# Kernel optimization log

Hardware: AMD Instinct MI355X
Metric: run time of the kernel (lower is better)

## Reference

```python
import jax, jax.numpy as jnp
import numpy as np

B, T, S, R, L = 16, 32, 512, 8, 256
H, E, V, NL = 512, 512, 50000, 3
OOV = 50


def setup_inputs() -> dict:
    key = jax.random.key(0)
    ks = jax.random.split(key, 40)
    p = lambda i, shape: jax.random.normal(ks[i], shape, dtype=jnp.float32) * 0.02
    d = {
        'tokens': jax.random.randint(ks[0], (B, T), 0, V),
        'src_oov': jax.random.randint(ks[1], (B, S), 0, V),
        'ref_oovs': jax.random.randint(ks[2], (B, R, L), 0, V),
        'src_mask': jnp.ones((B, S), bool),
        'ref_word_mask': jnp.ones((B, R, L), bool),
        'ref_doc_mask': jnp.ones((B, R), bool),
        'max_num_oov': OOV,
        'cur_word_rep': jax.random.normal(ks[3], (B, S, H), dtype=jnp.float32),
        'ref_word_reps': jax.random.normal(ks[4], (B, R, L, H), dtype=jnp.float32),
        'ref_doc_reps': jax.random.normal(ks[5], (B, R, H), dtype=jnp.float32),
        'hidden0': jax.random.normal(ks[6], (NL, B, H), dtype=jnp.float32),
        'embed_w': p(7, (V, E)),
        'gru_wih': p(8, (NL, 3 * H, H)),  # layer0 input dim E == H
        'gru_whh': p(9, (NL, 3 * H, H)),
        'gru_bih': p(10, (NL, 3 * H)),
        'gru_bhh': p(11, (NL, 3 * H)),
        'attn_Wd': p(12, (H, H)), 'attn_We': p(13, (H, H)), 'attn_v': p(14, (H,)),
        'hd_Wd': p(15, (H, H)), 'hd_We': p(16, (H, H)), 'hd_v': p(17, (H,)),
        'hw_Wd': p(18, (H, H)), 'hw_We': p(19, (H, H)), 'hw_v': p(20, (H,)),
        'gate_w': p(21, (2 * H, 1)), 'gate_b': p(22, (1,)),
        'fc_w': p(23, (2 * H, H)), 'fc_b': p(24, (H,)),
        'out_w': p(25, (H, V)), 'out_b': p(26, (V,)),
        'pgen_w': p(27, (E + 2 * H, 3)), 'pgen_b': p(28, (3,)),
    }
    return d


def _forward(embed_w, gru_wih, gru_whh, gru_bih, gru_bhh,
             attn_Wd, attn_We, attn_v, hd_Wd, hd_We, hd_v, hw_Wd, hw_We, hw_v,
             gate_w, gate_b, fc_w, fc_b, out_w, out_b, pgen_w, pgen_b,
             cur_word_rep, ref_word_reps, ref_doc_reps, hidden0,
             tokens, src_oov, ref_oovs, src_mask, ref_word_mask, ref_doc_mask,
             max_num_oov):
    b, t = tokens.shape
    x = embed_w[tokens]                               # [B,T,E]
    enc_proj = cur_word_rep @ attn_We                 # [B,S,H]
    doc_proj = ref_doc_reps @ hd_We                   # [B,R,H]
    word_proj = ref_word_reps @ hw_We                 # [B,R,L,H]
    NEG = jnp.float32(-1e9)

    def step(hidden, x_t):
        inp = x_t
        hs = []
        for l in range(hidden.shape[0]):
            gx = inp @ gru_wih[l].T + gru_bih[l]
            gh = hidden[l] @ gru_whh[l].T + gru_bhh[l]
            xr, xz, xn = jnp.split(gx, 3, -1)
            hr, hz, hn = jnp.split(gh, 3, -1)
            r = jax.nn.sigmoid(xr + hr)
            z = jax.nn.sigmoid(xz + hz)
            n = jnp.tanh(xn + r * hn)
            h = (1.0 - z) * n + z * hidden[l]
            hs.append(h)
            inp = h
        new_hidden = jnp.stack(hs)
        h_top = hs[-1]                                # [B,H]
        # additive attention over source words
        sc = jnp.tanh(enc_proj + (h_top @ attn_Wd)[:, None, :]) @ attn_v  # [B,S]
        aw = jax.nn.softmax(jnp.where(src_mask, sc, NEG), -1)
        ctx = jnp.einsum('bs,bsh->bh', aw, cur_word_rep)
        # hierarchical attention: doc level then word level
        scd = jnp.tanh(doc_proj + (h_top @ hd_Wd)[:, None, :]) @ hd_v     # [B,R]
        ad = jax.nn.softmax(jnp.where(ref_doc_mask, scd, NEG), -1)
        scw = jnp.tanh(word_proj + (h_top @ hw_Wd)[:, None, None, :]) @ hw_v  # [B,R,L]
        aww = jax.nn.softmax(jnp.where(ref_word_mask, scw, NEG), -1)
        ra = ad[:, :, None] * aww                     # [B,R,L]
        rctx = jnp.einsum('brl,brlh->bh', ra, ref_word_reps)
        # fusion gate
        g = jax.nn.sigmoid(jnp.concatenate([ctx, rctx], -1) @ gate_w + gate_b)  # [B,1]
        context = g * ctx + (1.0 - g) * rctx
        return new_hidden, (context, h_top, aw, ra)

    _, (contexts, hiddens, attn_dists, ref_attn_dists) = jax.lax.scan(
        step, hidden0, jnp.swapaxes(x, 0, 1))
    contexts = jnp.swapaxes(contexts, 0, 1)           # [B,T,H]
    hiddens = jnp.swapaxes(hiddens, 0, 1)             # [B,T,H]
    attn_dists = jnp.swapaxes(attn_dists, 0, 1)       # [B,T,S]
    ref_attn_dists = jnp.swapaxes(ref_attn_dists, 0, 1)  # [B,T,R,L]

    ch = jnp.concatenate([contexts, hiddens], -1)
    vocab_dist = jax.nn.softmax((ch @ fc_w + fc_b) @ out_w + out_b, -1)  # [B,T,V]
    pg = jax.nn.softmax(jnp.concatenate([contexts, hiddens, x], -1) @ pgen_w + pgen_b, -1)  # [B,T,3]
    vocab_dist_ = pg[..., 0:1] * vocab_dist
    attn_ = pg[..., 1:2] * attn_dists
    final = jnp.concatenate(
        [vocab_dist_, jnp.zeros((b, t, max_num_oov), vocab_dist_.dtype)], -1)
    bi = jnp.arange(b)[:, None, None]
    ti = jnp.arange(t)[None, :, None]
    idx = jnp.broadcast_to(src_oov[:, None, :], (b, t, src_oov.shape[-1]))
    final = final.at[bi, ti, idx].add(attn_)
    # multi-doc copy
    r, l = ref_oovs.shape[1], ref_oovs.shape[2]
    ref_attn_ = pg[..., 2][:, :, None, None] * ref_attn_dists
    ridx = jnp.broadcast_to(ref_oovs.reshape(b, 1, r * l), (b, t, r * l))
    final = final.at[bi, ti, ridx].add(ref_attn_.reshape(b, t, r * l))
    return final, attn_dists


def reference(tokens, src_oov, ref_oovs, src_mask, ref_word_mask, ref_doc_mask,
              max_num_oov, cur_word_rep, ref_word_reps, ref_doc_reps, hidden0,
              embed_w, gru_wih, gru_whh, gru_bih, gru_bhh,
              attn_Wd, attn_We, attn_v, hd_Wd, hd_We, hd_v, hw_Wd, hw_We, hw_v,
              gate_w, gate_b, fc_w, fc_b, out_w, out_b, pgen_w, pgen_b):
    return _forward(embed_w, gru_wih, gru_whh, gru_bih, gru_bhh,
                    attn_Wd, attn_We, attn_v, hd_Wd, hd_We, hd_v,
                    hw_Wd, hw_We, hw_v, gate_w, gate_b, fc_w, fc_b,
                    out_w, out_b, pgen_w, pgen_b,
                    cur_word_rep, ref_word_reps, ref_doc_reps, hidden0,
                    tokens, src_oov, ref_oovs, src_mask, ref_word_mask,
                    ref_doc_mask, max_num_oov)
```

## Files before the change

kernel.cpp:

```cpp
#include <hip/hip_runtime.h>
#include <hip/hip_bf16.h>


#define B_   16
#define T_   32
#define S_   512
#define R_   8
#define L_   256
#define RL_  2048
#define H_   512
#define V_   50000
#define NL_  3
#define OOV_ 50
#define M_   512
#define FINW 50050
#define S2C  2.8853900817779268f
#define GRUB 128
#define NCONV 128
#define HP16 520

typedef __attribute__((ext_vector_type(8))) short    short8;
typedef __attribute__((ext_vector_type(4))) float    f32x4;
typedef __attribute__((ext_vector_type(2))) _Float16 h2;
typedef __attribute__((ext_vector_type(8))) _Float16 h8;
// ... 265 lines not shown
  int cg = nb + cbase;
  long gbase = (long)(mb + rl) * FINW + cg;
  float mp = -1e30f;
  #pragma unroll 8
  for (int k = 0; k < 64; k += 2){
    float x0 = cbuf[rl][cbase + k], x1 = cbuf[rl][cbase + k + 1];
    float2 xy; xy.x = x0; xy.y = x1;
    *(float2*)(fin + gbase + k) = xy;
    if (cg + k < N)     mp = fmaxf(mp, x0);
    if (cg + k + 1 < N) mp = fmaxf(mp, x1);
  }
  float sp = 0.f;
  #pragma unroll 8
  for (int k = 0; k < 64; k++){
    if (cg + k < N) sp += __expf(cbuf[rl][cbase + k] - mp);
  }
  smx[rl][ch] = mp; ssx[rl][ch] = sp;
  __syncthreads();
  if (tid < 128){
    float ma = smx[tid][0], mb2 = smx[tid][1];
    float M = fmaxf(ma, mb2);
    float S = ssx[tid][0] * __expf(ma - M) + ssx[tid][1] * __expf(mb2 - M);
    long row = mb + tid;
    pm[row * 392 + blockIdx.y] = M;
    ps[row * 392 + blockIdx.y] = S;
  }
}


__global__ __launch_bounds__(512) void k_gru_mega(
    const float* __restrict__ gx0, const u16* __restrict__ wih_h,
    const u16* __restrict__ whh_h, const float* __restrict__ bih,
    const float* __restrict__ bhh, const float* __restrict__ hidden0,
    float* __restrict__ h_all, u16* __restrict__ ch_bf, unsigned int* cnt,
    const float* __restrict__ out_w, u16* __restrict__ outwT,
    const u16* __restrict__ cwr_bf, const u16* __restrict__ rwr_bf,
    const u16* __restrict__ rdr_bf, const u16* __restrict__ WT,
    u16* __restrict__ enc_bf, u16* __restrict__ wp_bf,
    float* __restrict__ doc_proj, int do_shadow){
  __shared__ u16 pH0[16][HP16], pH1[16][HP16], pX1[16][HP16], pH2[16][HP16], pX2[16][HP16];
  __shared__ float red0[8][3][4][16];
  __shared__ float red1[8][6][4][16];
  __shared__ float red2[8][6][4][16];
  __shared__ float tconv[2][32][33];
  int bid = blockIdx.x;
  int tid = threadIdx.x;

  if (bid >= GRUB){
    if (!do_shadow) return;
    int wid = bid - GRUB;
    int half = tid >> 8, t256 = tid & 255;
    int worker = wid * 2 + half;
    for (int tile = worker; tile < 1284; tile += 256){
      if (tile < 256)
        dev_gemm_tile(cwr_bf, H_, WT, H_, (const float*)0, (void*)enc_bf, H_,
                      H_, H_, 1, S2C, tile >> 2, tile & 3, t256);
      else if (tile < 1280){
        int t = tile - 256;
        dev_gemm_tile(rwr_bf, H_, WT + 2 * H_ * H_, H_, (const float*)0, (void*)wp_bf, H_,
                      H_, H_, 1, S2C, t >> 2, t & 3, t256);
      } else
        dev_gemm_tile(rdr_bf, H_, WT + H_ * H_, H_, (const float*)0, (void*)doc_proj, H_,
                      H_, H_, 0, S2C, 0, tile - 1280, t256);
    }
    __syncthreads();
    int sub = half, tx = t256 & 31, ty = t256 >> 5;
    const int NT = 1563 * 16;
    for (int base = wid * 2; base < NT; base += NCONV * 2){
      int tile = base + sub;
      bool act = tile < NT;
      int cx = act ? (tile % 1563) : 0;
      int ry = act ? (tile / 1563) : 0;
      int c0 = cx * 32, r0 = ry * 32;
      if (act){
        for (int i = ty; i < 32; i += 8){
          int c = c0 + tx;
          tconv[sub][i][tx] = (c < V_) ? out_w[(long)(r0 + i) * V_ + c] : 0.f;
        }
      }
      __syncthreads();
      if (act){
        for (int i = ty; i < 32; i += 8){
          int c = c0 + i;
          if (c < V_) outwT[(long)c * H_ + r0 + tx] = f2bf(tconv[sub][tx][i]);
        }
      }
      __syncthreads();
    }
    return;
  }

  int bx = bid;
  int b = tid & 15, jj = (tid >> 4) & 3, ks = tid >> 6;
  int j = bx * 4 + jj;
  int kbase = ks * 64;
  int srow = tid >> 5, sl32 = tid & 31;

  for (int s = 0; s < T_ + NL_ - 1; s++){
    int t0 = s, t1 = s - 1, t2v = s - 2;
    bool a0 = (t0 < T_);
    bool a1 = (t1 >= 0 && t1 < T_);
    bool a2 = (t2v >= 0 && t2v < T_);
    float hpj_r = 0.f, gx_r0 = 0.f, gx_r1 = 0.f, gx_r2 = 0.f;
    if (tid < 192){
      int lz = tid >> 6, b2 = tid & 15, jj2 = (tid >> 4) & 3;
      int j2 = bx * 4 + jj2;
      int tt = s - lz;
      if (tt >= 0 && tt < T_){
        hpj_r = (tt == 0) ? hidden0[(lz * B_ + b2) * H_ + j2]
                          : allcf(h_all + (long)((lz * T_ + tt - 1) * B_ + b2) * H_ + j2);
        if (lz == 0){
          const float* g = gx0 + (long)(b2 * T_ + tt) * 1536 + j2;
          gx_r0 = g[0]; gx_r1 = g[512]; gx_r2 = g[1024];
        }
      }
    }
    {
      u64 v;
      #define STAGE(PAN, ROWPTR, ATOMIC)                                         \
        {                                                                        \
          const u64* p = (const u64*)(ROWPTR);                                   \
          _Pragma("unroll")                                                      \
          for (int q = 0; q < 8; q++){                                           \
            v = (ATOMIC) ? allc(p + sl32 + 32 * q) : p[sl32 + 32 * q];           \
            union { u64 w; float f[2]; } uu; uu.w = v;                           \
            union { _Float16 h[2]; u32 u; } pk;                                  \
            pk.h[0] = (_Float16)uu.f[0]; pk.h[1] = (_Float16)uu.f[1];            \
            *(u32*)&PAN[srow][2 * (sl32 + 32 * q)] = pk.u;                       \
          }                                                                      \
        }
      if (a0){
        if (t0 == 0) STAGE(pH0, hidden0 + (long)(0 * B_ + srow) * H_, false)
        else         STAGE(pH0, h_all + (long)((0 * T_ + t0 - 1) * B_ + srow) * H_, true)
      }
      if (a1){
        if (t1 == 0) STAGE(pH1, hidden0 + (long)(1 * B_ + srow) * H_, false)
        else         STAGE(pH1, h_all + (long)((1 * T_ + t1 - 1) * B_ + srow) * H_, true)
        STAGE(pX1, h_all + (long)((0 * T_ + t1) * B_ + srow) * H_, true)
      }
      if (a2){
        if (t2v == 0) STAGE(pH2, hidden0 + (long)(2 * B_ + srow) * H_, false)
        else          STAGE(pH2, h_all + (long)((2 * T_ + t2v - 1) * B_ + srow) * H_, true)
        STAGE(pX2, h_all + (long)((1 * T_ + t2v) * B_ + srow) * H_, true)
      }
      #undef STAGE
    }
    __syncthreads();

    if (a0){
      const u16* wl = whh_h;
      const h8* w0 = (const h8*)(wl + ((long)(0 * H_ + j)) * H_ + kbase);
      const h8* w1 = (const h8*)(wl + ((long)(1 * H_ + j)) * H_ + kbase);
      const h8* w2 = (const h8*)(wl + ((long)(2 * H_ + j)) * H_ + kbase);
      float s0 = 0.f, s1 = 0.f, s2 = 0.f;
      #pragma unroll 2
      for (int k8 = 0; k8 < 8; k8++){
        h8 hv = *(const h8*)&pH0[b][kbase + 8 * k8];
        s0 = dot8h(w0[k8], hv, s0);
        s1 = dot8h(w1[k8], hv, s1);
        s2 = dot8h(w2[k8], hv, s2);
      }
      red0[ks][0][jj][b] = s0; red0[ks][1][jj][b] = s1; red0[ks][2][jj][b] = s2;
    }
    if (a1){
      const u16* wl = whh_h + (long)1 * 1536 * H_;
      const u16* ul = wih_h + (long)1 * 1536 * H_;
      const h8* w0 = (const h8*)(wl + ((long)(0 * H_ + j)) * H_ + kbase);
      const h8* w1 = (const h8*)(wl + ((long)(1 * H_ + j)) * H_ + kbase);
      const h8* w2 = (const h8*)(wl + ((long)(2 * H_ + j)) * H_ + kbase);
      const h8* u0 = (const h8*)(ul + ((long)(0 * H_ + j)) * H_ + kbase);
      const h8* u1 = (const h8*)(ul + ((long)(1 * H_ + j)) * H_ + kbase);
      const h8* u2 = (const h8*)(ul + ((long)(2 * H_ + j)) * H_ + kbase);
      float s0 = 0.f, s1 = 0.f, s2 = 0.f, x0 = 0.f, x1 = 0.f, x2 = 0.f;
      #pragma unroll 2
      for (int k8 = 0; k8 < 8; k8++){
        h8 hv = *(const h8*)&pH1[b][kbase + 8 * k8];
        h8 xv = *(const h8*)&pX1[b][kbase + 8 * k8];
        s0 = dot8h(w0[k8], hv, s0);
        s1 = dot8h(w1[k8], hv, s1);
        s2 = dot8h(w2[k8], hv, s2);
        x0 = dot8h(u0[k8], xv, x0);
        x1 = dot8h(u1[k8], xv, x1);
        x2 = dot8h(u2[k8], xv, x2);
      }
      red1[ks][0][jj][b] = s0; red1[ks][1][jj][b] = s1; red1[ks][2][jj][b] = s2;
      red1[ks][3][jj][b] = x0; red1[ks][4][jj][b] = x1; red1[ks][5][jj][b] = x2;
    }
    if (a2){
      const u16* wl = whh_h + (long)2 * 1536 * H_;
      const u16* ul = wih_h + (long)2 * 1536 * H_;
      const h8* w0 = (const h8*)(wl + ((long)(0 * H_ + j)) * H_ + kbase);
      const h8* w1 = (const h8*)(wl + ((long)(1 * H_ + j)) * H_ + kbase);
      const h8* w2 = (const h8*)(wl + ((long)(2 * H_ + j)) * H_ + kbase);
      const h8* u0 = (const h8*)(ul + ((long)(0 * H_ + j)) * H_ + kbase);
      const h8* u1 = (const h8*)(ul + ((long)(1 * H_ + j)) * H_ + kbase);
      const h8* u2 = (const h8*)(ul + ((long)(2 * H_ + j)) * H_ + kbase);
      float s0 = 0.f, s1 = 0.f, s2 = 0.f, x0 = 0.f, x1 = 0.f, x2 = 0.f;
      #pragma unroll 2
      for (int k8 = 0; k8 < 8; k8++){
        h8 hv = *(const h8*)&pH2[b][kbase + 8 * k8];
        h8 xv = *(const h8*)&pX2[b][kbase + 8 * k8];
        s0 = dot8h(w0[k8], hv, s0);
        s1 = dot8h(w1[k8], hv, s1);
        s2 = dot8h(w2[k8], hv, s2);
        x0 = dot8h(u0[k8], xv, x0);
        x1 = dot8h(u1[k8], xv, x1);
        x2 = dot8h(u2[k8], xv, x2);
      }
      red2[ks][0][jj][b] = s0; red2[ks][1][jj][b] = s1; red2[ks][2][jj][b] = s2;
      red2[ks][3][jj][b] = x0; red2[ks][4][jj][b] = x1; red2[ks][5][jj][b] = x2;
    }
    __syncthreads();

    if (tid < 192){
      int lz = tid >> 6, b2 = tid & 15, jj2 = (tid >> 4) & 3;
      int j2 = bx * 4 + jj2;
      int tt = s - lz;
      if (tt >= 0 && tt < T_){
        float gh[3], gxv[3];
        #pragma unroll
        for (int g = 0; g < 3; g++){
          float a = 0.f, c = 0.f;
          if (lz == 0){
            #pragma unroll
            for (int q = 0; q < 8; q++) a += red0[q][g][jj2][b2];
          } else if (lz == 1){
            #pragma unroll
            for (int q = 0; q < 8; q++){ a += red1[q][g][jj2][b2]; c += red1[q][3 + g][jj2][b2]; }
          } else {
            #pragma unroll
            for (int q = 0; q < 8; q++){ a += red2[q][g][jj2][b2]; c += red2[q][3 + g][jj2][b2]; }
          }
          gh[g] = a + bhh[lz * 1536 + g * H_ + j2];
          if (lz == 0) gxv[g] = (g == 0) ? gx_r0 : (g == 1) ? gx_r1 : gx_r2;
          else         gxv[g] = c + bih[lz * 1536 + g * H_ + j2];
        }
        float r = sigmoid_(gxv[0] + gh[0]);
        float z = sigmoid_(gxv[1] + gh[1]);
        float n = tanh_(gxv[2] + r * gh[2]);
        float h = (1.f - z) * n + z * hpj_r;
        union { float f; u32 u; } cv; cv.f = h;
        __hip_atomic_store((u32*)(h_all + (long)((lz * T_ + tt) * B_ + b2) * H_ + j2),
                           cv.u, __ATOMIC_RELAXED, __HIP_MEMORY_SCOPE_AGENT);
        if (lz == 2) ch_bf[(long)(b2 * T_ + tt) * 1024 + 512 + j2] = f2bf(h);
      }
    }
    if (s == T_ + NL_ - 2) break;

    __syncthreads();
    if (tid == 0)
      __hip_atomic_store(cnt + bx * 16, (u32)(s + 1),
                         __ATOMIC_RELAXED, __HIP_MEMORY_SCOPE_AGENT);
    if (tid < GRUB){
      long guard = 0;
      while (__hip_atomic_load(cnt + tid * 16, __ATOMIC_RELAXED, __HIP_MEMORY_SCOPE_AGENT)
               < (u32)(s + 1) && guard < (1L << 23)){
        __builtin_amdgcn_s_sleep(1);
        guard++;
      }
    }
    __syncthreads();
  }
}


__global__ __launch_bounds__(256) void k_scores2(const u16* __restrict__ enc,
    const u16* __restrict__ wp, const float* __restrict__ dec_all,
    const float* __restrict__ av, const float* __restrict__ wv,
    float* __restrict__ aw, float* __restrict__ ra){
  int b = blockIdx.x, y = blockIdx.y, tz = blockIdx.z;
  const u16* ebf; int erpb, doff, et, ldo; const float* vv; float* out;
  if (y < 8){ ebf = enc; erpb = S_;  doff = 0;    vv = av; out = aw; ldo = S_;  et = y; }
  else      { ebf = wp;  erpb = RL_; doff = 1024; vv = wv; out = ra; ldo = RL_; et = y - 8; }
  int tid = threadIdx.x;
  __shared__ float dsh[8][512];
  __shared__ float vsh[512];
  __shared__ float redsv[4];
  for (int i = tid; i < 8 * 128; i += 256){
    int tl = i >> 7, c = (i & 127) << 2;
    *(f32x4*)&dsh[tl][c] =
      *(const f32x4*)(dec_all + ((long)(b * T_) + tz * 8 + tl) * 1536 + doff + c);
  }
  for (int i = tid; i < 128; i += 256)
    *(f32x4*)&vsh[i << 2] = *(const f32x4*)(vv + (i << 2));
  __syncthreads();
  float pvv = vsh[tid] + vsh[tid + 256];
  for (int o = 32; o > 0; o >>= 1) pvv += __shfl_xor(pvv, o);
  if ((tid & 63) == 0) redsv[tid >> 6] = pvv;
  __syncthreads();
// ... 71 lines not shown
    if (tid == 0){
      float m = -1e30f;
      for (int q = 0; q < 8; q++) m = fmaxf(m, red8[q][0]);
      float e[8], sum = 0.f;
      for (int q = 0; q < 8; q++){ e[q] = __expf(red8[q][0] - m); sum += e[q]; }
      float inv = 1.f / sum;
      for (int q = 0; q < 8; q++) ad[rid * R_ + q] = e[q] * inv;
    }
  }
}

__global__ __launch_bounds__(256) void k_aww_ra(float* __restrict__ raBuf,
                                                const float* __restrict__ ad){
  int rid = blockIdx.x, r = blockIdx.y, tid = threadIdx.x;
  float* row = raBuf + (long)rid * RL_ + r * L_;
  float x = row[tid];
  float m = x;
  for (int o = 32; o > 0; o >>= 1) m = fmaxf(m, __shfl_xor(m, o));
  __shared__ float red[4];
  if ((tid & 63) == 0) red[tid >> 6] = m;
  __syncthreads();
  m = fmaxf(fmaxf(red[0], red[1]), fmaxf(red[2], red[3]));
  float e = __expf(x - m);
  float s = e;
  for (int o = 32; o > 0; o >>= 1) s += __shfl_xor(s, o);
  __syncthreads();
  if ((tid & 63) == 0) red[tid >> 6] = s;
  __syncthreads();
  s = red[0] + red[1] + red[2] + red[3];
  row[tid] = (e / s) * ad[rid * R_ + r];
}


__global__ __launch_bounds__(256) void k_awgemm(const float* __restrict__ wts, int KS, int CH,
    const u16* __restrict__ Wbuf, float* __restrict__ pdst){
  int b = blockIdx.x, ht = blockIdx.y, kc = blockIdx.z;
  int tid = threadIdx.x;
  int hl = tid & 63, tq = tid >> 6;
  int h = ht * 256 + hl * 4;
  int base = kc * CH;
  float a[8][4];
  #pragma unroll
  for (int tt = 0; tt < 8; tt++)
    #pragma unroll
    for (int q = 0; q < 4; q++) a[tt][q] = 0.f;
  const float* wrow = wts + ((long)(b * T_) + tq * 8) * KS + base;
  for (int sl = 0; sl < CH; sl++){
    const u16* wp = Wbuf + ((long)b * KS + base + sl) * H_ + h;
    u32 p0 = *(const u32*)(wp);
    u32 p1 = *(const u32*)(wp + 2);
    float v0 = bf2f((u16)(p0 & 0xffff)), v1 = bf2f((u16)(p0 >> 16));
    float v2 = bf2f((u16)(p1 & 0xffff)), v3 = bf2f((u16)(p1 >> 16));
    #pragma unroll
    for (int tt = 0; tt < 8; tt++){
      float w = wrow[(long)tt * KS + sl];
      a[tt][0] += w * v0; a[tt][1] += w * v1;
      a[tt][2] += w * v2; a[tt][3] += w * v3;
    }
  }
  #pragma unroll
  for (int tt = 0; tt < 8; tt++){
    long o = (long)kc * (2 * M_ * H_) + ((long)(b * T_ + tq * 8 + tt)) * H_ + h;
    *(f32x4*)(pdst + o) = (f32x4){a[tt][0], a[tt][1], a[tt][2], a[tt][3]};
  }
}

__global__ __launch_bounds__(256) void k_red8(const float* __restrict__ pbuf,
                                              float* __restrict__ outp){
  long n = 2L * M_ * H_;
// ... 28 lines not shown
    contexts[(long)rid * H_ + h] = v;
    ch_bf[(long)rid * 1024 + h] = f2bf(v);
  }
  float p0 = 0.f, p1 = 0.f, p2 = 0.f;
  for (int k = tid; k < 1536; k += 256){
    float v;
    if (k < 512)       v = g * c[k] + (1.f - g) * rc[k];
    else if (k < 1024) v = h_all[((2 * T_ + t) * B_ + b) * H_ + (k - 512)];
    else               v = bf2f(x_bf[(long)rid * H_ + (k - 1024)]);
    p0 += v * pgen_w[k * 3 + 0];
    p1 += v * pgen_w[k * 3 + 1];
    p2 += v * pgen_w[k * 3 + 2];
  }
  for (int o = 32; o > 0; o >>= 1){
    p0 += __shfl_xor(p0, o); p1 += __shfl_xor(p1, o); p2 += __shfl_xor(p2, o);
  }
  __shared__ float r0[4], r1[4], r2[4];
  if ((tid & 63) == 0){ r0[tid >> 6] = p0; r1[tid >> 6] = p1; r2[tid >> 6] = p2; }
  __syncthreads();
  if (tid == 0){
    p0 = r0[0]+r0[1]+r0[2]+r0[3] + pgen_b[0];
    p1 = r1[0]+r1[1]+r1[2]+r1[3] + pgen_b[1];
    p2 = r2[0]+r2[1]+r2[2]+r2[3] + pgen_b[2];
    float m = fmaxf(p0, fmaxf(p1, p2));
    float e0 = __expf(p0 - m), e1 = __expf(p1 - m), e2 = __expf(p2 - m);
    float inv = 1.f / (e0 + e1 + e2);
    pg[rid * 3 + 0] = e0 * inv;
    pg[rid * 3 + 1] = e1 * inv;
    pg[rid * 3 + 2] = e2 * inv;
  }
}


__global__ __launch_bounds__(256) void k_vred391(const float* __restrict__ pm,
    const float* __restrict__ ps, float* __restrict__ vmax, float* __restrict__ vsum){
  int rid = blockIdx.x, tid = threadIdx.x;
  const float* mrow = pm + (long)rid * 392;
  const float* srow = ps + (long)rid * 392;
  float m = -1e30f, s = 0.f;
  for (int q = tid; q < 391; q += 256){
    float m2 = mrow[q], s2 = srow[q];
    float M = fmaxf(m, m2);
    s = s * __expf(m - M) + s2 * __expf(m2 - M);
    m = M;
  }
  for (int o = 32; o > 0; o >>= 1){
    float m2 = __shfl_xor(m, o), s2 = __shfl_xor(s, o);
    float M = fmaxf(m, m2);
    s = s * __expf(m - M) + s2 * __expf(m2 - M);
    m = M;
  }
  __shared__ float rm[4], rs[4];
  if ((tid & 63) == 0){ rm[tid >> 6] = m; rs[tid >> 6] = s; }
  __syncthreads();
  if (tid == 0){
    float Mx = rm[0], Sx = rs[0];
    for (int q = 1; q < 4; q++){
      float M2 = fmaxf(Mx, rm[q]);
      Sx = Sx * __expf(Mx - M2) + rs[q] * __expf(rm[q] - M2);
      Mx = M2;
    }
    vmax[rid] = Mx; vsum[rid] = Sx;
  }
}

__global__ __launch_bounds__(256) void k_final_vocab(float* __restrict__ fin,
    const float* __restrict__ vmax, const float* __restrict__ vsum,
    const float* __restrict__ pg){
  int rid = blockIdx.y;
  int v = (blockIdx.x * 256 + threadIdx.x) * 2;
  if (v >= FINW) return;
  long base = (long)rid * FINW;
  float scale = pg[rid * 3 + 0] / vsum[rid];
  float mx = vmax[rid];
  if (v + 1 < V_){
    float2* p = (float2*)(fin + base + v);
    float2 x = *p;
    x.x = __expf(x.x - mx) * scale;
    x.y = __expf(x.y - mx) * scale;
    *p = x;
  } else {
    for (int q = 0; q < 2 && v + q < FINW; q++){
      float x = fin[base + v + q];
      fin[base + v + q] = (v + q < V_) ? __expf(x - mx) * scale : 0.f;
    }
  }
}

__global__ __launch_bounds__(256) void k_scatter_src(float* __restrict__ fin,
    const float* __restrict__ aw, const float* __restrict__ pg,
    const int* __restrict__ src_oov){
  int rid = blockIdx.x, tid = threadIdx.x;
  int b = rid / T_;
  float p1 = pg[rid * 3 + 1];
  for (int s = tid; s < S_; s += 256){
    float val = p1 * aw[(long)rid * S_ + s];
    int idx = src_oov[b * S_ + s];
    atomicAdd(fin + (long)rid * FINW + idx, val);
  }
}

__global__ __launch_bounds__(256) void k_scatter_ref(float* __restrict__ fin,
    const float* __restrict__ raBuf, const float* __restrict__ pg,
    const int* __restrict__ ref_oovs){
  int rid = blockIdx.x, tid = threadIdx.x;
  int b = rid / T_;
  float p2 = pg[rid * 3 + 2];
  for (int i = tid; i < RL_; i += 256){
    float val = p2 * raBuf[(long)rid * RL_ + i];
    int idx = ref_oovs[b * RL_ + i];
    atomicAdd(fin + (long)rid * FINW + idx, val);
  }
}


extern "C" void kernel_launch(void* const* d_in, const int* in_sizes, int n_in,
                              void* d_out, int out_size, void* d_ws, size_t ws_size,
                              hipStream_t stream)
{
  (void)in_sizes; (void)n_in; (void)out_size;
  const int*   tokens   = (const int*)  d_in[0];
  const int*   src_oov  = (const int*)  d_in[1];
  const int*   ref_oovs = (const int*)  d_in[2];
  const float* cwr      = (const float*)d_in[7];
  const float* rwr      = (const float*)d_in[8];
  const float* rdr      = (const float*)d_in[9];
  const float* hidden0  = (const float*)d_in[10];
  const float* embed_w  = (const float*)d_in[11];
  const float* gru_wih  = (const float*)d_in[12];
  const float* gru_whh  = (const float*)d_in[13];
  const float* gru_bih  = (const float*)d_in[14];
  const float* gru_bhh  = (const float*)d_in[15];
  const float* attn_Wd  = (const float*)d_in[16];
  const float* attn_We  = (const float*)d_in[17];
  const float* attn_v   = (const float*)d_in[18];
  const float* hd_Wd    = (const float*)d_in[19];
  const float* hd_We    = (const float*)d_in[20];
  const float* hd_v     = (const float*)d_in[21];
  const float* hw_Wd    = (const float*)d_in[22];
  const float* hw_We    = (const float*)d_in[23];
  const float* hw_v     = (const float*)d_in[24];
  const float* gate_w   = (const float*)d_in[25];
  const float* gate_b   = (const float*)d_in[26];
  const float* fc_w     = (const float*)d_in[27];
  const float* fc_b     = (const float*)d_in[28];
  const float* out_w    = (const float*)d_in[29];
  const float* out_b    = (const float*)d_in[30];
  const float* pgen_w   = (const float*)d_in[31];
  const float* pgen_b   = (const float*)d_in[32];

  float* fin = (float*)d_out;
  float* aw  = fin + (long)M_ * FINW;

  char* wptr = (char*)d_ws;
  auto alloc = [&](size_t nbytes) -> void* {
    void* p = (void*)wptr;
    wptr += (nbytes + 255) & ~(size_t)255;
    return p;
  };
  float* gx0      = (float*)alloc((size_t)M_ * 1536 * 4);
  float* h_all    = (float*)alloc((size_t)NL_ * T_ * B_ * H_ * 4);
  float* dec_all  = (float*)alloc((size_t)M_ * 1536 * 4);
  float* raBuf    = (float*)alloc((size_t)M_ * RL_ * 4);
  float* ad       = (float*)alloc((size_t)M_ * R_ * 4);
  float* ctx      = (float*)alloc((size_t)M_ * H_ * 4);
  float* rctx     = (float*)alloc((size_t)M_ * H_ * 4);
  float* contexts = (float*)alloc((size_t)M_ * H_ * 4);
  float* pg       = (float*)alloc((size_t)M_ * 3 * 4);
  float* vmax     = (float*)alloc((size_t)M_ * 4);
  float* vsum     = (float*)alloc((size_t)M_ * 4);
  float* pm       = (float*)alloc((size_t)M_ * 392 * 4);
  float* ps       = (float*)alloc((size_t)M_ * 392 * 4);
  float* doc_proj = (float*)alloc((size_t)B_ * R_ * H_ * 4);
  float* pbuf     = (float*)alloc((size_t)8 * 2 * M_ * H_ * 4);
  unsigned int* gru_cnt = (unsigned int*)alloc(GRUB * 16 * 4);
  u16* x_bf       = (u16*)alloc((size_t)M_ * H_ * 2);
  u16* ch_bf      = (u16*)alloc((size_t)M_ * 1024 * 2);
  u16* whh_h16    = (u16*)alloc((size_t)NL_ * 1536 * H_ * 2);
  u16* wih_h16    = (u16*)alloc((size_t)NL_ * 1536 * H_ * 2);
  u16* wih0_bf    = (u16*)alloc((size_t)1536 * H_ * 2);
  u16* WT         = (u16*)alloc((size_t)6 * H_ * H_ * 2);
  u16* fcwT       = (u16*)alloc((size_t)H_ * 1024 * 2);
  u16* fcout_bf   = (u16*)alloc((size_t)M_ * H_ * 2);
  u16* cwr_bf     = (u16*)alloc((size_t)B_ * S_ * H_ * 2);
  u16* enc_bf     = (u16*)alloc((size_t)B_ * S_ * H_ * 2);
  u16* rwr_bf     = (u16*)alloc((size_t)B_ * RL_ * H_ * 2);
  u16* wp_bf      = (u16*)alloc((size_t)B_ * RL_ * H_ * 2);
  u16* rdr_bf     = (u16*)alloc((size_t)B_ * R_ * H_ * 2);
  u16* outwT_ded  = (u16*)alloc((size_t)V_ * H_ * 2);
  bool big = ((char*)outwT_ded + (size_t)V_ * H_ * 2) <= ((char*)d_ws + ws_size);
  u16* outwT = big ? outwT_ded : rwr_bf;
  int nshadow = big ? NCONV : 0;

  hipMemsetAsync(gru_cnt, 0, GRUB * 16 * 4, stream);

  k_embed<<<M_, 256, 0, stream>>>(tokens, embed_w, x_bf);
  {
    CJ j0{cwr, cwr_bf, (long)B_ * S_ * H_, 0};
    CJ j1{rwr, rwr_bf, (long)B_ * RL_ * H_, 0};
    CJ j2{gru_whh, whh_h16, (long)NL_ * 1536 * H_, 1};
    CJ j3{gru_wih, wih_h16, (long)NL_ * 1536 * H_, 1};
    CJ j4{rdr, rdr_bf, (long)B_ * R_ * H_, 0};
    CJ j5{gru_wih, wih0_bf, (long)1536 * H_, 0};
    k_conv6<<<dim3(512, 6), 256, 0, stream>>>(j0, j1, j2, j3, j4, j5);
  }
  k_convT6<<<dim3(16, 16, 6), 256, 0, stream>>>(attn_We, hd_We, hw_We,
                                                attn_Wd, hd_Wd, hw_Wd, WT);
  k_convT<<<dim3(16, 32), 256, 0, stream>>>(fc_w, 1024, H_, fcwT);

  k_gemm_nt<<<dim3(4, 12), 256, 0, stream>>>(x_bf, H_, wih0_bf, H_, gru_bih,
                                             (void*)gx0, 1536, 1536, H_, 0, 1.f);
  if (!big){
    k_gemm_nt<<<dim3(64, 4), 256, 0, stream>>>(cwr_bf, H_, WT, H_, (const float*)0,
                                               (void*)enc_bf, H_, H_, H_, 1, S2C);
    k_gemm_nt<<<dim3(256, 4), 256, 0, stream>>>(rwr_bf, H_, WT + 2 * H_ * H_, H_, (const float*)0,
                                                (void*)wp_bf, H_, H_, H_, 1, S2C);
    k_gemm_nt<<<dim3(1, 4), 256, 0, stream>>>(rdr_bf, H_, WT + H_ * H_, H_, (const float*)0,
                                              (void*)doc_proj, H_, H_, H_, 0, S2C);
  }

  k_gru_mega<<<GRUB + nshadow, 512, 0, stream>>>(gx0, wih_h16, whh_h16, gru_bih, gru_bhh,
                                                 hidden0, h_all, ch_bf, gru_cnt,
                                                 out_w, outwT, cwr_bf, rwr_bf, rdr_bf,
                                                 WT, enc_bf, wp_bf, doc_proj, big ? 1 : 0);

  k_gemm_nt<<<dim3(4, 12), 256, 0, stream>>>(ch_bf + 512, 1024, WT + 3 * H_ * H_, H_,
                                             (const float*)0, (void*)dec_all, 1536, 1536, H_, 0, S2C);

  k_scores2<<<dim3(16, 40, 4), 256, 0, stream>>>(enc_bf, wp_bf, dec_all, attn_v, hw_v, aw, raBuf);
  k_smax_scd<<<dim3(M_, 2), 256, 0, stream>>>(aw, doc_proj, dec_all, hd_v, ad);
  k_aww_ra<<<dim3(M_, R_), 256, 0, stream>>>(raBuf, ad);

  k_awgemm<<<dim3(B_, 2, 8), 256, 0, stream>>>(aw, S_, 64, cwr_bf, pbuf);
  k_awgemm<<<dim3(B_, 2, 8), 256, 0, stream>>>(raBuf, RL_, 256, rwr_bf, pbuf + (long)M_ * H_);
  if (!big)
    k_convT<<<dim3(1563, 16), 256, 0, stream>>>(out_w, H_, V_, outwT);
  k_red8<<<(2 * M_ * H_ + 255) / 256, 256, 0, stream>>>(pbuf, ctx);

  k_gatepgen<<<M_, 256, 0, stream>>>(ctx, rctx, gate_w, gate_b, contexts, ch_bf,
                                     h_all, x_bf, pgen_w, pgen_b, pg);

  k_gemm_nt<<<dim3(4, 4), 256, 0, stream>>>(ch_bf, 1024, fcwT, 1024, fc_b,
                                            (void*)fcout_bf, H_, H_, 1024, 1, 1.f);
  k_gemm_out<<<dim3(4, 391), 256, 0, stream>>>(fcout_bf, outwT, out_b, fin, pm, ps);
  k_vred391<<<M_, 256, 0, stream>>>(pm, ps, vmax, vsum);
  k_final_vocab<<<dim3(98, M_), 256, 0, stream>>>(fin, vmax, vsum, pg);
  k_scatter_src<<<M_, 256, 0, stream>>>(fin, aw, pg, src_oov);
  k_scatter_ref<<<M_, 256, 0, stream>>>(fin, raBuf, pg, ref_oovs);
}
```

Before: 1.148 ms.

## Restructure GRU megakernel reduction, stage fp16 hidden states, and fuse tail kernels

The GRU persistent kernel now stores an fp16 copy of each hidden state so the next step can stage it into LDS without converting, and it reuses the layer-below panel as the input operand. The split-K reduction moves from a shared-memory reduce plus a second barrier to warp shuffles, and the biases are hoisted into registers. Each polling thread now checks two counters instead of one. Separately, the two awgemm launches are merged into one, vocab max/sum reduction is folded into k_final_vocab (each of its 98 blocks per row recomputes the reduction), and the two scatter kernels are merged. These changes cut per-step barrier and conversion latency on the recurrent critical path and reduce launch count, at the cost of redundant reductions and extra fp16 stores.

```diff
diff --git a/kernel.cpp b/kernel.cpp
--- a/kernel.cpp
+++ b/kernel.cpp
@@ -321,16 +321,14 @@
     const float* __restrict__ gx0, const u16* __restrict__ wih_h,
     const u16* __restrict__ whh_h, const float* __restrict__ bih,
     const float* __restrict__ bhh, const float* __restrict__ hidden0,
-    float* __restrict__ h_all, u16* __restrict__ ch_bf, unsigned int* cnt,
+    float* __restrict__ h_all, u16* __restrict__ h16,
+    u16* __restrict__ ch_bf, unsigned int* cnt,
     const float* __restrict__ out_w, u16* __restrict__ outwT,
     const u16* __restrict__ cwr_bf, const u16* __restrict__ rwr_bf,
     const u16* __restrict__ rdr_bf, const u16* __restrict__ WT,
     u16* __restrict__ enc_bf, u16* __restrict__ wp_bf,
     float* __restrict__ doc_proj, int do_shadow){
-  __shared__ u16 pH0[16][HP16], pH1[16][HP16], pX1[16][HP16], pH2[16][HP16], pX2[16][HP16];
-  __shared__ float red0[8][3][4][16];
-  __shared__ float red1[8][6][4][16];
-  __shared__ float red2[8][6][4][16];
+  __shared__ u16 P0[16][HP16], P1[16][HP16], P2[16][HP16];
   __shared__ float tconv[2][32][33];
   int bid = blockIdx.x;
   int tid = threadIdx.x;
@@ -380,76 +378,109 @@
   }
 
   int bx = bid;
-  int b = tid & 15, jj = (tid >> 4) & 3, ks = tid >> 6;
+  int jj = tid >> 7, b = (tid >> 3) & 15, ks = tid & 7;
   int j = bx * 4 + jj;
   int kbase = ks * 64;
   int srow = tid >> 5, sl32 = tid & 31;
+
+  float bh00 = 0, bh01 = 0, bh02 = 0, bh10 = 0, bh11 = 0, bh12 = 0,
+        bh20 = 0, bh21 = 0, bh22 = 0, bi10 = 0, bi11 = 0, bi12 = 0,
+        bi20 = 0, bi21 = 0, bi22 = 0;
+  if (ks == 0){
+    bh00 = bhh[0 * 1536 + 0 * H_ + j]; bh01 = bhh[0 * 1536 + 1 * H_ + j];
+    bh02 = bhh[0 * 1536 + 2 * H_ + j];
+    bh10 = bhh[1 * 1536 + 0 * H_ + j]; bh11 = bhh[1 * 1536 + 1 * H_ + j];
+    bh12 = bhh[1 * 1536 + 2 * H_ + j];
+    bh20 = bhh[2 * 1536 + 0 * H_ + j]; bh21 = bhh[2 * 1536 + 1 * H_ + j];
+    bh22 = bhh[2 * 1536 + 2 * H_ + j];
+    bi10 = bih[1 * 1536 + 0 * H_ + j]; bi11 = bih[1 * 1536 + 1 * H_ + j];
+    bi12 = bih[1 * 1536 + 2 * H_ + j];
+    bi20 = bih[2 * 1536 + 0 * H_ + j]; bi21 = bih[2 * 1536 + 1 * H_ + j];
+    bi22 = bih[2 * 1536 + 2 * H_ + j];
+  }
 
   for (int s = 0; s < T_ + NL_ - 1; s++){
     int t0 = s, t1 = s - 1, t2v = s - 2;
     bool a0 = (t0 < T_);
     bool a1 = (t1 >= 0 && t1 < T_);
     bool a2 = (t2v >= 0 && t2v < T_);
-    float hpj_r = 0.f, gx_r0 = 0.f, gx_r1 = 0.f, gx_r2 = 0.f;
-    if (tid < 192){
-      int lz = tid >> 6, b2 = tid & 15, jj2 = (tid >> 4) & 3;
-      int j2 = bx * 4 + jj2;
-      int tt = s - lz;
-      if (tt >= 0 && tt < T_){
-        hpj_r = (tt == 0) ? hidden0[(lz * B_ + b2) * H_ + j2]
-                          : allcf(h_all + (long)((lz * T_ + tt - 1) * B_ + b2) * H_ + j2);
-        if (lz == 0){
-          const float* g = gx0 + (long)(b2 * T_ + tt) * 1536 + j2;
-          gx_r0 = g[0]; gx_r1 = g[512]; gx_r2 = g[1024];
+    float hp0 = 0.f, hp1 = 0.f, hp2 = 0.f, g0r = 0.f, g1r = 0.f, g2r = 0.f;
+    if (ks == 0){
+      if (a0){
+        hp0 = (t0 == 0) ? hidden0[(0 * B_ + b) * H_ + j]
+                        : allcf(h_all + (long)((0 * T_ + t0 - 1) * B_ + b) * H_ + j);
+        const float* g = gx0 + (long)(b * T_ + t0) * 1536 + j;
+        g0r = g[0]; g1r = g[512]; g2r = g[1024];
+      }
+      if (a1) hp1 = (t1 == 0) ? hidden0[(1 * B_ + b) * H_ + j]
+                              : allcf(h_all + (long)((1 * T_ + t1 - 1) * B_ + b) * H_ + j);
+      if (a2) hp2 = (t2v == 0) ? hidden0[(2 * B_ + b) * H_ + j]
+                               : allcf(h_all + (long)((2 * T_ + t2v - 1) * B_ + b) * H_ + j);
+    }
+    if (a0 && t0 == 0){
+      const f32x4* p = (const f32x4*)(hidden0 + (long)(0 * B_ + srow) * H_);
+      #pragma unroll
+      for (int q = 0; q < 4; q++){
+        f32x4 v = p[sl32 + 32 * q];
+        u64 pk = (u64)f2h(v[0]) | ((u64)f2h(v[1]) << 16)
+               | ((u64)f2h(v[2]) << 32) | ((u64)f2h(v[3]) << 48);
+        *(u64*)&P0[srow][4 * (sl32 + 32 * q)] = pk;
+      }
+    } else if (a0 || a1){
+      const u64* p = (const u64*)(h16 + ((long)(0 * T_ + s - 1) * B_ + srow) * H_);
+      #pragma unroll
+      for (int q = 0; q < 4; q++)
+        *(u64*)&P0[srow][4 * (sl32 + 32 * q)] = allc(p + sl32 + 32 * q);
+    }
+    if (a1 && t1 == 0){
+      const f32x4* p = (const f32x4*)(hidden0 + (long)(1 * B_ + srow) * H_);
+      #pragma unroll
+      for (int q = 0; q < 4; q++){
+        f32x4 v = p[sl32 + 32 * q];
+        u64 pk = (u64)f2h(v[0]) | ((u64)f2h(v[1]) << 16)
+               | ((u64)f2h(v[2]) << 32) | ((u64)f2h(v[3]) << 48);
+        *(u64*)&P1[srow][4 * (sl32 + 32 * q)] = pk;
+      }
+    } else if (a1 || a2){
+      const u64* p = (const u64*)(h16 + ((long)(1 * T_ + s - 2) * B_ + srow) * H_);
+      #pragma unroll
+      for (int q = 0; q < 4; q++)
+        *(u64*)&P1[srow][4 * (sl32 + 32 * q)] = allc(p + sl32 + 32 * q);
+    }
+    if (a2){
+      if (t2v == 0){
+        const f32x4* p = (const f32x4*)(hidden0 + (long)(2 * B_ + srow) * H_);
+        #pragma unroll
+        for (int q = 0; q < 4; q++){
+          f32x4 v = p[sl32 + 32 * q];
+          u64 pk = (u64)f2h(v[0]) | ((u64)f2h(v[1]) << 16)
+                 | ((u64)f2h(v[2]) << 32) | ((u64)f2h(v[3]) << 48);
+          *(u64*)&P2[srow][4 * (sl32 + 32 * q)] = pk;
         }
-      }
-    }
-    {
-      u64 v;
-      #define STAGE(PAN, ROWPTR, ATOMIC)                                         \
-        {                                                                        \
-          const u64* p = (const u64*)(ROWPTR);                                   \
-          _Pragma("unroll")                                                      \
-          for (int q = 0; q < 8; q++){                                           \
-            v = (ATOMIC) ? allc(p + sl32 + 32 * q) : p[sl32 + 32 * q];           \
-            union { u64 w; float f[2]; } uu; uu.w = v;                           \
-            union { _Float16 h[2]; u32 u; } pk;                                  \
-            pk.h[0] = (_Float16)uu.f[0]; pk.h[1] = (_Float16)uu.f[1];            \
-            *(u32*)&PAN[srow][2 * (sl32 + 32 * q)] = pk.u;                       \
-          }                                                                      \
-        }
-      if (a0){
-        if (t0 == 0) STAGE(pH0, hidden0 + (long)(0 * B_ + srow) * H_, false)
-        else         STAGE(pH0, h_all + (long)((0 * T_ + t0 - 1) * B_ + srow) * H_, true)
-      }
-      if (a1){
-        if (t1 == 0) STAGE(pH1, hidden0 + (long)(1 * B_ + srow) * H_, false)
-        else         STAGE(pH1, h_all + (long)((1 * T_ + t1 - 1) * B_ + srow) * H_, true)
-        STAGE(pX1, h_all + (long)((0 * T_ + t1) * B_ + srow) * H_, true)
-      }
-      if (a2){
-        if (t2v == 0) STAGE(pH2, hidden0 + (long)(2 * B_ + srow) * H_, false)
-        else          STAGE(pH2, h_all + (long)((2 * T_ + t2v - 1) * B_ + srow) * H_, true)
-        STAGE(pX2, h_all + (long)((1 * T_ + t2v) * B_ + srow) * H_, true)
-      }
-      #undef STAGE
+      } else {
+        const u64* p = (const u64*)(h16 + ((long)(2 * T_ + s - 3) * B_ + srow) * H_);
+        #pragma unroll
+        for (int q = 0; q < 4; q++)
+          *(u64*)&P2[srow][4 * (sl32 + 32 * q)] = allc(p + sl32 + 32 * q);
+      }
     }
     __syncthreads();
 
+    float A0 = 0, A1 = 0, A2 = 0;
+    float Bh0 = 0, Bh1 = 0, Bh2 = 0, Bx0 = 0, Bx1 = 0, Bx2 = 0;
+    float Ch0 = 0, Ch1 = 0, Ch2 = 0, Cx0 = 0, Cx1 = 0, Cx2 = 0;
     if (a0){
       const u16* wl = whh_h;
       const h8* w0 = (const h8*)(wl + ((long)(0 * H_ + j)) * H_ + kbase);
       const h8* w1 = (const h8*)(wl + ((long)(1 * H_ + j)) * H_ + kbase);
       const h8* w2 = (const h8*)(wl + ((long)(2 * H_ + j)) * H_ + kbase);
-      float s0 = 0.f, s1 = 0.f, s2 = 0.f;
       #pragma unroll 2
       for (int k8 = 0; k8 < 8; k8++){
-        h8 hv = *(const h8*)&pH0[b][kbase + 8 * k8];
-        s0 = dot8h(w0[k8], hv, s0);
-        s1 = dot8h(w1[k8], hv, s1);
-        s2 = dot8h(w2[k8], hv, s2);
-      }
-      red0[ks][0][jj][b] = s0; red0[ks][1][jj][b] = s1; red0[ks][2][jj][b] = s2;
+        h8 hv = *(const h8*)&P0[b][kbase + 8 * k8];
+        A0 = dot8h(w0[k8], hv, A0);
+        A1 = dot8h(w1[k8], hv, A1);
+        A2 = dot8h(w2[k8], hv, A2);
+      }
     }
     if (a1){
       const u16* wl = whh_h + (long)1 * 1536 * H_;
@@ -460,20 +491,17 @@
       const h8* u0 = (const h8*)(ul + ((long)(0 * H_ + j)) * H_ + kbase);
       const h8* u1 = (const h8*)(ul + ((long)(1 * H_ + j)) * H_ + kbase);
       const h8* u2 = (const h8*)(ul + ((long)(2 * H_ + j)) * H_ + kbase);
-      float s0 = 0.f, s1 = 0.f, s2 = 0.f, x0 = 0.f, x1 = 0.f, x2 = 0.f;
       #pragma unroll 2
       for (int k8 = 0; k8 < 8; k8++){
-        h8 hv = *(const h8*)&pH1[b][kbase + 8 * k8];
-        h8 xv = *(const h8*)&pX1[b][kbase + 8 * k8];
-        s0 = dot8h(w0[k8], hv, s0);
-        s1 = dot8h(w1[k8], hv, s1);
-        s2 = dot8h(w2[k8], hv, s2);
-        x0 = dot8h(u0[k8], xv, x0);
-        x1 = dot8h(u1[k8], xv, x1);
-        x2 = dot8h(u2[k8], xv, x2);
-      }
-      red1[ks][0][jj][b] = s0; red1[ks][1][jj][b] = s1; red1[ks][2][jj][b] = s2;
-      red1[ks][3][jj][b] = x0; red1[ks][4][jj][b] = x1; red1[ks][5][jj][b] = x2;
+        h8 hv = *(const h8*)&P1[b][kbase + 8 * k8];
+        h8 xv = *(const h8*)&P0[b][kbase + 8 * k8];
+        Bh0 = dot8h(w0[k8], hv, Bh0);
+        Bh1 = dot8h(w1[k8], hv, Bh1);
+        Bh2 = dot8h(w2[k8], hv, Bh2);
+        Bx0 = dot8h(u0[k8], xv, Bx0);
+        Bx1 = dot8h(u1[k8], xv, Bx1);
+        Bx2 = dot8h(u2[k8], xv, Bx2);
+      }
     }
     if (a2){
       const u16* wl = whh_h + (long)2 * 1536 * H_;
@@ -484,54 +512,58 @@
       const h8* u0 = (const h8*)(ul + ((long)(0 * H_ + j)) * H_ + kbase);
       const h8* u1 = (const h8*)(ul + ((long)(1 * H_ + j)) * H_ + kbase);
       const h8* u2 = (const h8*)(ul + ((long)(2 * H_ + j)) * H_ + kbase);
-      float s0 = 0.f, s1 = 0.f, s2 = 0.f, x0 = 0.f, x1 = 0.f, x2 = 0.f;
       #pragma unroll 2
       for (int k8 = 0; k8 < 8; k8++){
-        h8 hv = *(const h8*)&pH2[b][kbase + 8 * k8];
-        h8 xv = *(const h8*)&pX2[b][kbase + 8 * k8];
-        s0 = dot8h(w0[k8], hv, s0);
-        s1 = dot8h(w1[k8], hv, s1);
-        s2 = dot8h(w2[k8], hv, s2);
-        x0 = dot8h(u0[k8], xv, x0);
-        x1 = dot8h(u1[k8], xv, x1);
-        x2 = dot8h(u2[k8], xv, x2);
-      }
-      red2[ks][0][jj][b] = s0; red2[ks][1][jj][b] = s1; red2[ks][2][jj][b] = s2;
-      red2[ks][3][jj][b] = x0; red2[ks][4][jj][b] = x1; red2[ks][5][jj][b] = x2;
-    }
-    __syncthreads();
-
-    if (tid < 192){
-      int lz = tid >> 6, b2 = tid & 15, jj2 = (tid >> 4) & 3;
-      int j2 = bx * 4 + jj2;
-      int tt = s - lz;
-      if (tt >= 0 && tt < T_){
-        float gh[3], gxv[3];
-        #pragma unroll
-        for (int g = 0; g < 3; g++){
-          float a = 0.f, c = 0.f;
-          if (lz == 0){
-            #pragma unroll
-            for (int q = 0; q < 8; q++) a += red0[q][g][jj2][b2];
-          } else if (lz == 1){
-            #pragma unroll
-            for (int q = 0; q < 8; q++){ a += red1[q][g][jj2][b2]; c += red1[q][3 + g][jj2][b2]; }
-          } else {
-            #pragma unroll
-            for (int q = 0; q < 8; q++){ a += red2[q][g][jj2][b2]; c += red2[q][3 + g][jj2][b2]; }
-          }
-          gh[g] = a + bhh[lz * 1536 + g * H_ + j2];
-          if (lz == 0) gxv[g] = (g == 0) ? gx_r0 : (g == 1) ? gx_r1 : gx_r2;
-          else         gxv[g] = c + bih[lz * 1536 + g * H_ + j2];
-        }
-        float r = sigmoid_(gxv[0] + gh[0]);
-        float z = sigmoid_(gxv[1] + gh[1]);
-        float n = tanh_(gxv[2] + r * gh[2]);
-        float h = (1.f - z) * n + z * hpj_r;
+        h8 hv = *(const h8*)&P2[b][kbase + 8 * k8];
+        h8 xv = *(const h8*)&P1[b][kbase + 8 * k8];
+        Ch0 = dot8h(w0[k8], hv, Ch0);
+        Ch1 = dot8h(w1[k8], hv, Ch1);
+        Ch2 = dot8h(w2[k8], hv, Ch2);
+        Cx0 = dot8h(u0[k8], xv, Cx0);
+        Cx1 = dot8h(u1[k8], xv, Cx1);
+        Cx2 = dot8h(u2[k8], xv, Cx2);
+      }
+    }
+    #define RED3(v) { v += __shfl_xor(v, 1); v += __shfl_xor(v, 2); v += __shfl_xor(v, 4); }
+    if (a0){ RED3(A0) RED3(A1) RED3(A2) }
+    if (a1){ RED3(Bh0) RED3(Bh1) RED3(Bh2) RED3(Bx0) RED3(Bx1) RED3(Bx2) }
+    if (a2){ RED3(Ch0) RED3(Ch1) RED3(Ch2) RED3(Cx0) RED3(Cx1) RED3(Cx2) }
+    #undef RED3
+
+    if (ks == 0){
+      if (a0){
+        float r = sigmoid_(g0r + A0 + bh00);
+        float z = sigmoid_(g1r + A1 + bh01);
+        float n = tanh_(g2r + r * (A2 + bh02));
+        float h = (1.f - z) * n + z * hp0;
         union { float f; u32 u; } cv; cv.f = h;
-        __hip_atomic_store((u32*)(h_all + (long)((lz * T_ + tt) * B_ + b2) * H_ + j2),
+        __hip_atomic_store((u32*)(h_all + (long)((0 * T_ + t0) * B_ + b) * H_ + j),
                            cv.u, __ATOMIC_RELAXED, __HIP_MEMORY_SCOPE_AGENT);
-        if (lz == 2) ch_bf[(long)(b2 * T_ + tt) * 1024 + 512 + j2] = f2bf(h);
+        __hip_atomic_store(h16 + ((long)(0 * T_ + t0) * B_ + b) * H_ + j,
+                           f2h(h), __ATOMIC_RELAXED, __HIP_MEMORY_SCOPE_AGENT);
+      }
+      if (a1){
+        float r = sigmoid_(Bx0 + bi10 + Bh0 + bh10);
+        float z = sigmoid_(Bx1 + bi11 + Bh1 + bh11);
+        float n = tanh_(Bx2 + bi12 + r * (Bh2 + bh12));
+        float h = (1.f - z) * n + z * hp1;
+        union { float f; u32 u; } cv; cv.f = h;
+        __hip_atomic_store((u32*)(h_all + (long)((1 * T_ + t1) * B_ + b) * H_ + j),
+                           cv.u, __ATOMIC_RELAXED, __HIP_MEMORY_SCOPE_AGENT);
+        __hip_atomic_store(h16 + ((long)(1 * T_ + t1) * B_ + b) * H_ + j,
+                           f2h(h), __ATOMIC_RELAXED, __HIP_MEMORY_SCOPE_AGENT);
+      }
+      if (a2){
+        float r = sigmoid_(Cx0 + bi20 + Ch0 + bh20);
+        float z = sigmoid_(Cx1 + bi21 + Ch1 + bh21);
+        float n = tanh_(Cx2 + bi22 + r * (Ch2 + bh22));
+        float h = (1.f - z) * n + z * hp2;
+        union { float f; u32 u; } cv; cv.f = h;
+        __hip_atomic_store((u32*)(h_all + (long)((2 * T_ + t2v) * B_ + b) * H_ + j),
+                           cv.u, __ATOMIC_RELAXED, __HIP_MEMORY_SCOPE_AGENT);
+        __hip_atomic_store(h16 + ((long)(2 * T_ + t2v) * B_ + b) * H_ + j,
+                           f2h(h), __ATOMIC_RELAXED, __HIP_MEMORY_SCOPE_AGENT);
+        ch_bf[(long)(b * T_ + t2v) * 1024 + 512 + j] = f2bf(h);
       }
     }
     if (s == T_ + NL_ - 2) break;
@@ -540,10 +572,12 @@
     if (tid == 0)
       __hip_atomic_store(cnt + bx * 16, (u32)(s + 1),
                          __ATOMIC_RELAXED, __HIP_MEMORY_SCOPE_AGENT);
-    if (tid < GRUB){
+    if (tid < 64){
       long guard = 0;
-      while (__hip_atomic_load(cnt + tid * 16, __ATOMIC_RELAXED, __HIP_MEMORY_SCOPE_AGENT)
-               < (u32)(s + 1) && guard < (1L << 23)){
+      while ((__hip_atomic_load(cnt + tid * 16, __ATOMIC_RELAXED, __HIP_MEMORY_SCOPE_AGENT)
+                < (u32)(s + 1) ||
+              __hip_atomic_load(cnt + (tid + 64) * 16, __ATOMIC_RELAXED, __HIP_MEMORY_SCOPE_AGENT)
+                < (u32)(s + 1)) && guard < (1L << 23)){
         __builtin_amdgcn_s_sleep(1);
         guard++;
       }
@@ -681,9 +715,13 @@
 }
 
 
-__global__ __launch_bounds__(256) void k_awgemm(const float* __restrict__ wts, int KS, int CH,
-    const u16* __restrict__ Wbuf, float* __restrict__ pdst){
-  int b = blockIdx.x, ht = blockIdx.y, kc = blockIdx.z;
+__global__ __launch_bounds__(256) void k_awgemm2(const float* __restrict__ aw,
+    const float* __restrict__ raBuf, const u16* __restrict__ cwr_bf,
+    const u16* __restrict__ rwr_bf, float* __restrict__ pbuf){
+  int b = blockIdx.x, ht = blockIdx.y, z = blockIdx.z;
+  const float* wts; const u16* Wbuf; float* pdst; int KS, CH, kc;
+  if (z < 8){ wts = aw;    Wbuf = cwr_bf; pdst = pbuf;                 KS = S_;  CH = 64;  kc = z; }
+  else      { wts = raBuf; Wbuf = rwr_bf; pdst = pbuf + (long)M_ * H_; KS = RL_; CH = 256; kc = z - 8; }
   int tid = threadIdx.x;
   int hl = tid & 63, tq = tid >> 6;
   int h = ht * 256 + hl * 4;
@@ -778,9 +816,10 @@
 }
 
 
-__global__ __launch_bounds__(256) void k_vred391(const float* __restrict__ pm,
-    const float* __restrict__ ps, float* __restrict__ vmax, float* __restrict__ vsum){
-  int rid = blockIdx.x, tid = threadIdx.x;
+__global__ __launch_bounds__(256) void k_final_vocab(float* __restrict__ fin,
+    const float* __restrict__ pm, const float* __restrict__ ps,
+    const float* __restrict__ pg){
+  int rid = blockIdx.y, tid = threadIdx.x;
   const float* mrow = pm + (long)rid * 392;
   const float* srow = ps + (long)rid * 392;
   float m = -1e30f, s = 0.f;
@@ -796,7 +835,7 @@
     s = s * __expf(m - M) + s2 * __expf(m2 - M);
     m = M;
   }
-  __shared__ float rm[4], rs[4];
+  __shared__ float rm[4], rs[4], fm, fs;
   if ((tid & 63) == 0){ rm[tid >> 6] = m; rs[tid >> 6] = s; }
   __syncthreads();
   if (tid == 0){
@@ -806,19 +845,14 @@
       Sx = Sx * __expf(Mx - M2) + rs[q] * __expf(rm[q] - M2);
       Mx = M2;
     }
-    vmax[rid] = Mx; vsum[rid] = Sx;
-  }
-}
-
-__global__ __launch_bounds__(256) void k_final_vocab(float* __restrict__ fin,
-    const float* __restrict__ vmax, const float* __restrict__ vsum,
-    const float* __restrict__ pg){
-  int rid = blockIdx.y;
-  int v = (blockIdx.x * 256 + threadIdx.x) * 2;
+    fm = Mx; fs = Sx;
+  }
+  __syncthreads();
+  float mx = fm;
+  float scale = pg[rid * 3 + 0] / fs;
+  int v = (blockIdx.x * 256 + tid) * 2;
   if (v >= FINW) return;
   long base = (long)rid * FINW;
-  float scale = pg[rid * 3 + 0] / vsum[rid];
-  float mx = vmax[rid];
   if (v + 1 < V_){
     float2* p = (float2*)(fin + base + v);
     float2 x = *p;
@@ -833,29 +867,27 @@
   }
 }
 
-__global__ __launch_bounds__(256) void k_scatter_src(float* __restrict__ fin,
-    const float* __restrict__ aw, const float* __restrict__ pg,
-    const int* __restrict__ src_oov){
-  int rid = blockIdx.x, tid = threadIdx.x;
-  int b = rid / T_;
-  float p1 = pg[rid * 3 + 1];
-  for (int s = tid; s < S_; s += 256){
-    float val = p1 * aw[(long)rid * S_ + s];
-    int idx = src_oov[b * S_ + s];
-    atomicAdd(fin + (long)rid * FINW + idx, val);
-  }
-}
-
-__global__ __launch_bounds__(256) void k_scatter_ref(float* __restrict__ fin,
-    const float* __restrict__ raBuf, const float* __restrict__ pg,
+__global__ __launch_bounds__(512) void k_scatter(float* __restrict__ fin,
+    const float* __restrict__ aw, const float* __restrict__ raBuf,
+    const float* __restrict__ pg, const int* __restrict__ src_oov,
     const int* __restrict__ ref_oovs){
   int rid = blockIdx.x, tid = threadIdx.x;
   int b = rid / T_;
-  float p2 = pg[rid * 3 + 2];
-  for (int i = tid; i < RL_; i += 256){
-    float val = p2 * raBuf[(long)rid * RL_ + i];
-    int idx = ref_oovs[b * RL_ + i];
-    atomicAdd(fin + (long)rid * FINW + idx, val);
+  if (tid < 256){
+    float p1 = pg[rid * 3 + 1];
+    for (int s = tid; s < S_; s += 256){
+      float val = p1 * aw[(long)rid * S_ + s];
+      int idx = src_oov[b * S_ + s];
+      atomicAdd(fin + (long)rid * FINW + idx, val);
+    }
+  } else {
+    int t2 = tid - 256;
+    float p2 = pg[rid * 3 + 2];
+    for (int i = t2; i < RL_; i += 256){
+      float val = p2 * raBuf[(long)rid * RL_ + i];
+      int idx = ref_oovs[b * RL_ + i];
+      atomicAdd(fin + (long)rid * FINW + idx, val);
+    }
   }
 }
 
@@ -913,13 +945,12 @@
   float* rctx     = (float*)alloc((size_t)M_ * H_ * 4);
   float* contexts = (float*)alloc((size_t)M_ * H_ * 4);
   float* pg       = (float*)alloc((size_t)M_ * 3 * 4);
-  float* vmax     = (float*)alloc((size_t)M_ * 4);
-  float* vsum     = (float*)alloc((size_t)M_ * 4);
   float* pm       = (float*)alloc((size_t)M_ * 392 * 4);
   float* ps       = (float*)alloc((size_t)M_ * 392 * 4);
   float* doc_proj = (float*)alloc((size_t)B_ * R_ * H_ * 4);
   float* pbuf     = (float*)alloc((size_t)8 * 2 * M_ * H_ * 4);
-  unsigned int* gru_cnt = (unsigned int*)alloc(GRUB * 16 * 4);
+  unsigned int* gru_cnt = (unsigned int*)alloc((GRUB + NCONV) * 16 * 4);
+  u16* h16        = (u16*)alloc((size_t)NL_ * T_ * B_ * H_ * 2);
   u16* x_bf       = (u16*)alloc((size_t)M_ * H_ * 2);
   u16* ch_bf      = (u16*)alloc((size_t)M_ * 1024 * 2);
   u16* whh_h16    = (u16*)alloc((size_t)NL_ * 1536 * H_ * 2);
@@ -938,7 +969,7 @@
   u16* outwT = big ? outwT_ded : rwr_bf;
   int nshadow = big ? NCONV : 0;
 
-  hipMemsetAsync(gru_cnt, 0, GRUB * 16 * 4, stream);
+  hipMemsetAsync(gru_cnt, 0, (GRUB + NCONV) * 16 * 4, stream);
 
   k_embed<<<M_, 256, 0, stream>>>(tokens, embed_w, x_bf);
   {
@@ -966,7 +997,7 @@
   }
 
   k_gru_mega<<<GRUB + nshadow, 512, 0, stream>>>(gx0, wih_h16, whh_h16, gru_bih, gru_bhh,
-                                                 hidden0, h_all, ch_bf, gru_cnt,
+                                                 hidden0, h_all, h16, ch_bf, gru_cnt,
                                                  out_w, outwT, cwr_bf, rwr_bf, rdr_bf,
                                                  WT, enc_bf, wp_bf, doc_proj, big ? 1 : 0);
 
@@ -977,8 +1008,7 @@
   k_smax_scd<<<dim3(M_, 2), 256, 0, stream>>>(aw, doc_proj, dec_all, hd_v, ad);
   k_aww_ra<<<dim3(M_, R_), 256, 0, stream>>>(raBuf, ad);
 
-  k_awgemm<<<dim3(B_, 2, 8), 256, 0, stream>>>(aw, S_, 64, cwr_bf, pbuf);
-  k_awgemm<<<dim3(B_, 2, 8), 256, 0, stream>>>(raBuf, RL_, 256, rwr_bf, pbuf + (long)M_ * H_);
+  k_awgemm2<<<dim3(B_, 2, 16), 256, 0, stream>>>(aw, raBuf, cwr_bf, rwr_bf, pbuf);
   if (!big)
     k_convT<<<dim3(1563, 16), 256, 0, stream>>>(out_w, H_, V_, outwT);
   k_red8<<<(2 * M_ * H_ + 255) / 256, 256, 0, stream>>>(pbuf, ctx);
@@ -989,8 +1019,6 @@
   k_gemm_nt<<<dim3(4, 4), 256, 0, stream>>>(ch_bf, 1024, fcwT, 1024, fc_b,
                                             (void*)fcout_bf, H_, H_, 1024, 1, 1.f);
   k_gemm_out<<<dim3(4, 391), 256, 0, stream>>>(fcout_bf, outwT, out_b, fin, pm, ps);
-  k_vred391<<<M_, 256, 0, stream>>>(pm, ps, vmax, vsum);
-  k_final_vocab<<<dim3(98, M_), 256, 0, stream>>>(fin, vmax, vsum, pg);
-  k_scatter_src<<<M_, 256, 0, stream>>>(fin, aw, pg, src_oov);
-  k_scatter_ref<<<M_, 256, 0, stream>>>(fin, raBuf, pg, ref_oovs);
-}
+  k_final_vocab<<<dim3(98, M_), 256, 0, stream>>>(fin, pm, ps, pg);
+  k_scatter<<<M_, 512, 0, stream>>>(fin, aw, raBuf, pg, src_oov, ref_oovs);
+}
```

Measured after the change: 1.754 ms. 1.53x slower.
